# Kernel optimization log

Measured on AMD Instinct MI355X. Metric: run time of the kernel, lower is better.

## Reference

```python
import jax, jax.numpy as jnp
import numpy as np

BATCH = 4096
DIM = 128
TEMP = 0.5


def setup_inputs() -> dict:
    key = jax.random.key(0)
    k1, k2 = jax.random.split(key)
    z_i = jax.random.normal(k1, (BATCH, DIM), dtype=jnp.float32)
    z_j = jax.random.normal(k2, (BATCH, DIM), dtype=jnp.float32)
    return {"z_i": z_i, "z_j": z_j}


def reference(z_i, z_j):
    B = z_i.shape[0]
    N = 2 * B
    z = jnp.concatenate([z_i, z_j], axis=0)  # [N, D]
    # cosine similarity = normalize then GEMM (instead of O(N^2*D) broadcast)
    zn = z / jnp.maximum(jnp.linalg.norm(z, axis=1, keepdims=True), 1e-8)
    sim = (zn @ zn.T) / TEMP  # [N, N]

    # positives: sim[i, i+B] and sim[i+B, i]
    pos = jnp.concatenate([jnp.diagonal(sim, B), jnp.diagonal(sim, -B)])  # [N]

    idx = jnp.arange(N)
    diag_mask = idx[:, None] == idx[None, :]
    pos_mask = (idx[:, None] == idx[None, :] + B) | (idx[:, None] + B == idx[None, :])
    neg_mask = ~(diag_mask | pos_mask)

    # CE with label 0 over logits [pos, negatives]:
    # loss_i = -pos_i + logsumexp({pos_i} U negatives_i)
    #        = -pos_i + logsumexp(sim_i over all j != i)   (pos pair is included once)
    lse = jax.nn.logsumexp(jnp.where(diag_mask, -jnp.inf, sim), axis=1)  # [N]
    loss = jnp.sum(lse - pos) / N

    # fraction of (row, negative) pairs with positive logit > negative logit,
    # divided by N twice as in the original code
    correct = jnp.sum(jnp.where(neg_mask, pos[:, None] > sim, False))
    acc = correct.astype(jnp.float32) / N / N
    return (loss, acc)
```

## Files before the change

kernel.cpp:

```cpp
#include <hip/hip_runtime.h>
#include <hip/hip_bf16.h>

#define NN 8192
#define DD 128
#define BB 4096

#define ROWS_PER_BLOCK 128
#define COLSPLIT 16
#define COLS_PER_BLOCK (NN / COLSPLIT)
#define TILES (COLS_PER_BLOCK / 64)

typedef __attribute__((ext_vector_type(8))) short short8;
typedef __attribute__((ext_vector_type(4))) float f32x4;

typedef __attribute__((address_space(3))) unsigned lds_u32;
typedef __attribute__((address_space(1))) unsigned glb_u32;

__global__ __launch_bounds__(128) void prep_kernel(
    const float* __restrict__ zi, const float* __restrict__ zj,
    __hip_bfloat16* __restrict__ zn, float* __restrict__ posh,
    float* __restrict__ sd, float* __restrict__ rowsum,
    int* __restrict__ rowcnt) {
  int r0 = blockIdx.x;
  int w = threadIdx.x >> 6;
  int lane = threadIdx.x & 63;
  int row = r0 + w * BB;
  const float* src = (w ? zj : zi) + (size_t)r0 * DD;
  float2 v = *reinterpret_cast<const float2*>(src + lane * 2);
  float ss = v.x * v.x + v.y * v.y;
  #pragma unroll
  for (int m = 1; m < 64; m <<= 1) ss += __shfl_xor(ss, m, 64);
  float inv = 1.0f / fmaxf(sqrtf(ss), 1e-8f);
  __hip_bfloat16 b0 = __float2bfloat16(v.x * inv);
  __hip_bfloat16 b1 = __float2bfloat16(v.y * inv);
  *reinterpret_cast<__hip_bfloat162*>(zn + (size_t)row * DD + lane * 2) =
      __hip_bfloat162{b0, b1};
  float f0 = __bfloat162float(b0), f1 = __bfloat162float(b1);
  float sq = f0 * f0 + f1 * f1;
  __shared__ float sb[2][DD];
  sb[w][2 * lane] = f0;
  sb[w][2 * lane + 1] = f1;
  __syncthreads();
  float o0 = sb[w ^ 1][2 * lane], o1 = sb[w ^ 1][2 * lane + 1];
  float dp = f0 * o0 + f1 * o1;
  #pragma unroll
  for (int m = 1; m < 64; m <<= 1) {
    sq += __shfl_xor(sq, m, 64);
    dp += __shfl_xor(dp, m, 64);
  }
  if (lane == 0) {
    sd[row] = sq;
    posh[row] = dp;
    rowsum[row] = 0.0f;
    rowcnt[row] = 0;
  }
}

__global__ __launch_bounds__(256) void main_kernel(
    const __hip_bfloat16* __restrict__ zn, const float* __restrict__ posh,
    float* __restrict__ rowsum, int* __restrict__ rowcnt) {
  __shared__ char ldsbuf[2][16384];

  const int tid = threadIdx.x;
  const int w = tid >> 6;
  const int lane = tid & 63;
  const int lo = lane & 15, hi = lane >> 4;
  const int rowBase = blockIdx.x * ROWS_PER_BLOCK;
  const int colBase = blockIdx.y * COLS_PER_BLOCK;
  const short* znS = reinterpret_cast<const short*>(zn);

  #define STAGE(bufidx, gcol0)                                               \
    {                                                                        \
      _Pragma("unroll")                                                      \
      for (int q = 0; q < 4; ++q) {                                          \
        int s_ = 4 * w + q;                                                  \
        int coll_ = 4 * s_ + (lane >> 4);                                    \
        int lc_ = (lane & 15) ^ (coll_ & 7);                                 \
        const short* src_ = znS + (size_t)((gcol0) + coll_) * DD + lc_ * 8;  \
        __builtin_amdgcn_global_load_lds(                                    \
            (const glb_u32*)src_, (lds_u32*)(&ldsbuf[bufidx][s_ * 1024]),    \
            16, 0, 0);                                                       \
      }                                                                      \
    }

  STAGE(0, colBase);

  short8 a[2][4];
  #pragma unroll
  for (int rf = 0; rf < 2; ++rf) {
    int arow = rowBase + 32 * w + 16 * rf + lo;
    const short* p = znS + (size_t)arow * DD + 8 * hi;
    #pragma unroll
    for (int c = 0; c < 4; ++c)
      a[rf][c] = *reinterpret_cast<const short8*>(p + 32 * c);
  }

  float posv[2][4];
  float sume[2][4];
  int cntv[2][4];
  #pragma unroll
  for (int rf = 0; rf < 2; ++rf)
    #pragma unroll
    for (int r = 0; r < 4; ++r) {
      posv[rf][r] = posh[rowBase + 32 * w + 16 * rf + 4 * hi + r];
      sume[rf][r] = 0.0f;
      cntv[rf][r] = 0;
    }

  __syncthreads();

  #pragma unroll 2
  for (int t = 0; t < TILES; ++t) {
    if (t + 1 < TILES) STAGE((t + 1) & 1, colBase + (t + 1) * 64);
    #pragma unroll
    for (int cf = 0; cf < 4; ++cf) {
      short8 b[4];
      #pragma unroll
      for (int c = 0; c < 4; ++c) {
        int coll = 16 * cf + lo;
        int off = coll * 256 + 16 * ((hi + 4 * c) ^ (lo & 7));
        b[c] = *reinterpret_cast<const short8*>(&ldsbuf[t & 1][off]);
      }
      #pragma unroll
      for (int rf = 0; rf < 2; ++rf) {
        f32x4 acc = {0.0f, 0.0f, 0.0f, 0.0f};
        #pragma unroll
        for (int c = 0; c < 4; ++c)
          acc = __builtin_amdgcn_mfma_f32_16x16x32_bf16(a[rf][c], b[c], acc,
                                                        0, 0, 0);
        #pragma unroll
        for (int r = 0; r < 4; ++r) {
          float s = acc[r];
          sume[rf][r] += exp2f(s * 2.885390082f);
          cntv[rf][r] += (posv[rf][r] > s) ? 1 : 0;
        }
      }
    }
    __syncthreads();
  }

  #pragma unroll
  for (int rf = 0; rf < 2; ++rf)
    #pragma unroll
    for (int r = 0; r < 4; ++r) {
      float v = sume[rf][r];
      int c2 = cntv[rf][r];
      #pragma unroll
      for (int m = 1; m < 16; m <<= 1) {
        v += __shfl_xor(v, m, 64);
        c2 += __shfl_xor(c2, m, 64);
      }
      if (lo == 0) {
        int row = rowBase + 32 * w + 16 * rf + 4 * hi + r;
        atomicAdd(&rowsum[row], v);
        atomicAdd(&rowcnt[row], c2);
      }
    }
}

__global__ __launch_bounds__(1024) void finalize_kernel(
    const float* __restrict__ rowsum, const int* __restrict__ rowcnt,
    const float* __restrict__ posh, const float* __restrict__ sd,
    float* __restrict__ out) {
  int tid = threadIdx.x;
  float lsum = 0.0f;
  unsigned csum = 0;
  #pragma unroll
  for (int k = 0; k < NN / 1024; ++k) {
    int i = tid + k * 1024;
    float diag = __expf(sd[i] + sd[i]);
    lsum += logf(rowsum[i] - diag) - 2.0f * posh[i];
    csum += (unsigned)rowcnt[i];
  }
  #pragma unroll
  for (int m = 1; m < 64; m <<= 1) {
    lsum += __shfl_xor(lsum, m, 64);
    csum += __shfl_xor(csum, m, 64);
  }
  __shared__ float ls[16];
  __shared__ unsigned cs[16];
  int w = tid >> 6, lane = tid & 63;
  if (lane == 0) { ls[w] = lsum; cs[w] = csum; }
  __syncthreads();
  if (tid == 0) {
    float L = 0.0f;
    unsigned long long C = 0;
    #pragma unroll
    for (int k = 0; k < 16; ++k) { L += ls[k]; C += cs[k]; }
    out[0] = L / (float)NN;
    out[1] = (float)((double)C / ((double)NN * (double)NN));
  }
}

extern "C" void kernel_launch(void* const* d_in, const int* in_sizes, int n_in,
                              void* d_out, int out_size, void* d_ws,
                              size_t ws_size, hipStream_t stream) {
  const float* zi = (const float*)d_in[0];
  const float* zj = (const float*)d_in[1];
  float* out = (float*)d_out;

  __hip_bfloat16* zn = (__hip_bfloat16*)d_ws;
  float* posh = (float*)((char*)d_ws + (size_t)NN * DD * 2);
  float* sd = posh + NN;
  float* rowsum = sd + NN;
  int* rowcnt = (int*)(rowsum + NN);

  prep_kernel<<<BB, 128, 0, stream>>>(zi, zj, zn, posh, sd, rowsum, rowcnt);
  main_kernel<<<dim3(NN / ROWS_PER_BLOCK, COLSPLIT), 256, 0, stream>>>(
      zn, posh, rowsum, rowcnt);
  finalize_kernel<<<1, 1024, 0, stream>>>(rowsum, rowcnt, posh, sd, out);
}
```

Measured before the change: 98.54 us.

## Fuse prep, main and finalize into one cooperative kernel with grid syncs

Merges the three launches into a single cooperative kernel that uses grid-wide barriers between the normalize, similarity/accumulate and finalize phases, with the old three-kernel path kept as a fallback. It also folds the 1/temperature and log2(e) scaling into the normalized vectors (the ALPHA factor) so the inner loop calls a raw hardware exp2 with no multiply. Prep now handles two rows per wave, using all 1024 blocks. This removes launch gaps and an inner-loop multiply, but grid syncs cost time and the cooperative launch needs all 1024 blocks to be resident at once. The bf16 rounding now applies to the scaled values, which slightly shifts precision.

```diff
diff --git a/kernel.cpp b/kernel.cpp
--- a/kernel.cpp
+++ b/kernel.cpp
@@ -1,5 +1,8 @@
 #include <hip/hip_runtime.h>
 #include <hip/hip_bf16.h>
+#include <hip/hip_cooperative_groups.h>
+
+namespace cg = cooperative_groups;
 
 #define NN 8192
 #define DD 128
@@ -9,6 +12,11 @@
 #define COLSPLIT 16
 #define COLS_PER_BLOCK (NN / COLSPLIT)
 #define TILES (COLS_PER_BLOCK / 64)
+#define GRID_X (NN / ROWS_PER_BLOCK)
+#define NBLOCKS (GRID_X * COLSPLIT)
+
+#define ALPHA 1.69864354f
+#define LN2 0.6931471805599453f
 
 typedef __attribute__((ext_vector_type(8))) short short8;
 typedef __attribute__((ext_vector_type(4))) float f32x4;
@@ -16,57 +24,79 @@
 typedef __attribute__((address_space(3))) unsigned lds_u32;
 typedef __attribute__((address_space(1))) unsigned glb_u32;
 
-__global__ __launch_bounds__(128) void prep_kernel(
+static __device__ __forceinline__ float fast_exp2(float x) {
+#if __has_builtin(__builtin_amdgcn_exp2f)
+  return __builtin_amdgcn_exp2f(x);
+#else
+  float r;
+  asm("v_exp_f32 %0, %1" : "=v"(r) : "v"(x));
+  return r;
+#endif
+}
+
+static __device__ __forceinline__ void prep_work(
     const float* __restrict__ zi, const float* __restrict__ zj,
     __hip_bfloat16* __restrict__ zn, float* __restrict__ posh,
     float* __restrict__ sd, float* __restrict__ rowsum,
-    int* __restrict__ rowcnt) {
-  int r0 = blockIdx.x;
-  int w = threadIdx.x >> 6;
-  int lane = threadIdx.x & 63;
-  int row = r0 + w * BB;
-  const float* src = (w ? zj : zi) + (size_t)r0 * DD;
-  float2 v = *reinterpret_cast<const float2*>(src + lane * 2);
-  float ss = v.x * v.x + v.y * v.y;
-  #pragma unroll
-  for (int m = 1; m < 64; m <<= 1) ss += __shfl_xor(ss, m, 64);
-  float inv = 1.0f / fmaxf(sqrtf(ss), 1e-8f);
-  __hip_bfloat16 b0 = __float2bfloat16(v.x * inv);
-  __hip_bfloat16 b1 = __float2bfloat16(v.y * inv);
-  *reinterpret_cast<__hip_bfloat162*>(zn + (size_t)row * DD + lane * 2) =
+    int* __restrict__ rowcnt, int bid) {
+  const int w = threadIdx.x >> 6;
+  const int lane = threadIdx.x & 63;
+  const int r = 4 * bid + w;
+  const float2 va =
+      *reinterpret_cast<const float2*>(zi + (size_t)r * DD + lane * 2);
+  const float2 vb =
+      *reinterpret_cast<const float2*>(zj + (size_t)r * DD + lane * 2);
+  float ssa = va.x * va.x + va.y * va.y;
+  float ssb = vb.x * vb.x + vb.y * vb.y;
+  #pragma unroll
+  for (int m = 1; m < 64; m <<= 1) {
+    ssa += __shfl_xor(ssa, m, 64);
+    ssb += __shfl_xor(ssb, m, 64);
+  }
+  const float ia = ALPHA / fmaxf(sqrtf(ssa), 1e-8f);
+  const float ib = ALPHA / fmaxf(sqrtf(ssb), 1e-8f);
+  __hip_bfloat16 a0 = __float2bfloat16(va.x * ia);
+  __hip_bfloat16 a1 = __float2bfloat16(va.y * ia);
+  __hip_bfloat16 b0 = __float2bfloat16(vb.x * ib);
+  __hip_bfloat16 b1 = __float2bfloat16(vb.y * ib);
+  *reinterpret_cast<__hip_bfloat162*>(zn + (size_t)r * DD + lane * 2) =
+      __hip_bfloat162{a0, a1};
+  *reinterpret_cast<__hip_bfloat162*>(zn + (size_t)(r + BB) * DD + lane * 2) =
       __hip_bfloat162{b0, b1};
-  float f0 = __bfloat162float(b0), f1 = __bfloat162float(b1);
-  float sq = f0 * f0 + f1 * f1;
-  __shared__ float sb[2][DD];
-  sb[w][2 * lane] = f0;
-  sb[w][2 * lane + 1] = f1;
-  __syncthreads();
-  float o0 = sb[w ^ 1][2 * lane], o1 = sb[w ^ 1][2 * lane + 1];
-  float dp = f0 * o0 + f1 * o1;
+  float fa0 = __bfloat162float(a0), fa1 = __bfloat162float(a1);
+  float fb0 = __bfloat162float(b0), fb1 = __bfloat162float(b1);
+  float sqa = fa0 * fa0 + fa1 * fa1;
+  float sqb = fb0 * fb0 + fb1 * fb1;
+  float dp = fa0 * fb0 + fa1 * fb1;
   #pragma unroll
   for (int m = 1; m < 64; m <<= 1) {
-    sq += __shfl_xor(sq, m, 64);
+    sqa += __shfl_xor(sqa, m, 64);
+    sqb += __shfl_xor(sqb, m, 64);
     dp += __shfl_xor(dp, m, 64);
   }
   if (lane == 0) {
-    sd[row] = sq;
-    posh[row] = dp;
-    rowsum[row] = 0.0f;
-    rowcnt[row] = 0;
-  }
-}
-
-__global__ __launch_bounds__(256) void main_kernel(
+    sd[r] = sqa;
+    sd[r + BB] = sqb;
+    posh[r] = dp;
+    posh[r + BB] = dp;
+    rowsum[r] = 0.0f;
+    rowsum[r + BB] = 0.0f;
+    rowcnt[r] = 0;
+    rowcnt[r + BB] = 0;
+  }
+}
+
+static __device__ __forceinline__ void main_work(
     const __hip_bfloat16* __restrict__ zn, const float* __restrict__ posh,
-    float* __restrict__ rowsum, int* __restrict__ rowcnt) {
+    float* __restrict__ rowsum, int* __restrict__ rowcnt, int bx, int by) {
   __shared__ char ldsbuf[2][16384];
 
   const int tid = threadIdx.x;
   const int w = tid >> 6;
   const int lane = tid & 63;
   const int lo = lane & 15, hi = lane >> 4;
-  const int rowBase = blockIdx.x * ROWS_PER_BLOCK;
-  const int colBase = blockIdx.y * COLS_PER_BLOCK;
+  const int rowBase = bx * ROWS_PER_BLOCK;
+  const int colBase = by * COLS_PER_BLOCK;
   const short* znS = reinterpret_cast<const short*>(zn);
 
   #define STAGE(bufidx, gcol0)                                               \
@@ -131,7 +161,7 @@
         #pragma unroll
         for (int r = 0; r < 4; ++r) {
           float s = acc[r];
-          sume[rf][r] += exp2f(s * 2.885390082f);
+          sume[rf][r] += fast_exp2(s);
           cntv[rf][r] += (posv[rf][r] > s) ? 1 : 0;
         }
       }
@@ -156,9 +186,10 @@
         atomicAdd(&rowcnt[row], c2);
       }
     }
-}
-
-__global__ __launch_bounds__(1024) void finalize_kernel(
+  #undef STAGE
+}
+
+static __device__ __forceinline__ void finalize_work(
     const float* __restrict__ rowsum, const int* __restrict__ rowcnt,
     const float* __restrict__ posh, const float* __restrict__ sd,
     float* __restrict__ out) {
@@ -166,10 +197,10 @@
   float lsum = 0.0f;
   unsigned csum = 0;
   #pragma unroll
-  for (int k = 0; k < NN / 1024; ++k) {
-    int i = tid + k * 1024;
-    float diag = __expf(sd[i] + sd[i]);
-    lsum += logf(rowsum[i] - diag) - 2.0f * posh[i];
+  for (int k = 0; k < NN / 256; ++k) {
+    int i = tid + k * 256;
+    float diag = fast_exp2(sd[i]);
+    lsum += logf(rowsum[i] - diag) - LN2 * posh[i];
     csum += (unsigned)rowcnt[i];
   }
   #pragma unroll
@@ -177,19 +208,52 @@
     lsum += __shfl_xor(lsum, m, 64);
     csum += __shfl_xor(csum, m, 64);
   }
-  __shared__ float ls[16];
-  __shared__ unsigned cs[16];
+  __shared__ float ls[4];
+  __shared__ unsigned cs[4];
   int w = tid >> 6, lane = tid & 63;
   if (lane == 0) { ls[w] = lsum; cs[w] = csum; }
   __syncthreads();
   if (tid == 0) {
-    float L = 0.0f;
-    unsigned long long C = 0;
-    #pragma unroll
-    for (int k = 0; k < 16; ++k) { L += ls[k]; C += cs[k]; }
+    float L = ls[0] + ls[1] + ls[2] + ls[3];
+    unsigned long long C =
+        (unsigned long long)cs[0] + cs[1] + cs[2] + cs[3];
     out[0] = L / (float)NN;
     out[1] = (float)((double)C / ((double)NN * (double)NN));
   }
+}
+
+__global__ __launch_bounds__(256, 4) void mono_kernel(
+    const float* __restrict__ zi, const float* __restrict__ zj,
+    __hip_bfloat16* __restrict__ zn, float* __restrict__ posh,
+    float* __restrict__ sd, float* __restrict__ rowsum,
+    int* __restrict__ rowcnt, float* __restrict__ out) {
+  const int bid = blockIdx.x + blockIdx.y * gridDim.x;
+  prep_work(zi, zj, zn, posh, sd, rowsum, rowcnt, bid);
+  cg::this_grid().sync();
+  main_work(zn, posh, rowsum, rowcnt, blockIdx.x, blockIdx.y);
+  cg::this_grid().sync();
+  if (bid == 0) finalize_work(rowsum, rowcnt, posh, sd, out);
+}
+
+__global__ __launch_bounds__(256) void prep_kernel(
+    const float* __restrict__ zi, const float* __restrict__ zj,
+    __hip_bfloat16* __restrict__ zn, float* __restrict__ posh,
+    float* __restrict__ sd, float* __restrict__ rowsum,
+    int* __restrict__ rowcnt) {
+  prep_work(zi, zj, zn, posh, sd, rowsum, rowcnt, blockIdx.x);
+}
+
+__global__ __launch_bounds__(256) void main_kernel(
+    const __hip_bfloat16* __restrict__ zn, const float* __restrict__ posh,
+    float* __restrict__ rowsum, int* __restrict__ rowcnt) {
+  main_work(zn, posh, rowsum, rowcnt, blockIdx.x, blockIdx.y);
+}
+
+__global__ __launch_bounds__(256) void finalize_kernel(
+    const float* __restrict__ rowsum, const int* __restrict__ rowcnt,
+    const float* __restrict__ posh, const float* __restrict__ sd,
+    float* __restrict__ out) {
+  finalize_work(rowsum, rowcnt, posh, sd, out);
 }
 
 extern "C" void kernel_launch(void* const* d_in, const int* in_sizes, int n_in,
@@ -205,8 +269,16 @@
   float* rowsum = sd + NN;
   int* rowcnt = (int*)(rowsum + NN);
 
-  prep_kernel<<<BB, 128, 0, stream>>>(zi, zj, zn, posh, sd, rowsum, rowcnt);
-  main_kernel<<<dim3(NN / ROWS_PER_BLOCK, COLSPLIT), 256, 0, stream>>>(
-      zn, posh, rowsum, rowcnt);
-  finalize_kernel<<<1, 1024, 0, stream>>>(rowsum, rowcnt, posh, sd, out);
-}
+  void* args[] = {(void*)&zi, (void*)&zj, (void*)&zn, (void*)&posh,
+                  (void*)&sd, (void*)&rowsum, (void*)&rowcnt, (void*)&out};
+  hipError_t err = hipLaunchCooperativeKernel(
+      (const void*)mono_kernel, dim3(GRID_X, COLSPLIT), dim3(256), args, 0,
+      stream);
+  if (err != hipSuccess) {
+    prep_kernel<<<NBLOCKS, 256, 0, stream>>>(zi, zj, zn, posh, sd, rowsum,
+                                             rowcnt);
+    main_kernel<<<dim3(GRID_X, COLSPLIT), 256, 0, stream>>>(zn, posh, rowsum,
+                                                            rowcnt);
+    finalize_kernel<<<1, 256, 0, stream>>>(rowsum, rowcnt, posh, sd, out);
+  }
+}
```

Result: slower. 296.0 us (+200.4%).
